# Kernel optimization log

Hardware: AMD Instinct MI355X
Metric: run time of the kernel (lower is better)

Reference implementation:

```python
import jax, jax.numpy as jnp
import numpy as np

B, S, D = 2, 1024, 2048
H, DN, DR, DV, R = 16, 128, 64, 128, 512
E, K, FI, SI = 12, 4, 1408, 2816
THETA = 10000.0
EPS = 1e-6


def rmsnorm(x, w):
    return x * jax.lax.rsqrt(jnp.mean(x * x, -1, keepdims=True) + EPS) * w


def rope(x, cos, sin):
    # interleaved-pair rotation (torch view_as_complex convention)
    x1, x2 = x[..., 0::2], x[..., 1::2]
    return jnp.stack([x1 * cos - x2 * sin, x1 * sin + x2 * cos], axis=-1).reshape(x.shape)


def setup_inputs() -> dict:
    key = jax.random.key(0)
    ks = jax.random.split(key, 16)
    w = lambda k, sh: jax.random.normal(k, sh, jnp.float32) * 0.02
    inp = {
        'x': jax.random.normal(ks[0], (B, S, D), jnp.float32),
        'wq': w(ks[1], (D, H * (DN + DR))),
        'wkv_a': w(ks[2], (D, R + DR)),
        'kv_norm_w': jnp.ones((R,), jnp.float32),
        'wkv_b': w(ks[3], (R, H * (DN + DV))),
        'wo': w(ks[4], (H * DV, D)),
        'norm_w': jnp.ones((D,), jnp.float32),
        'gate_w': w(ks[5], (D, E)),
        'gate_b': jnp.zeros((E,), jnp.float32),
        'w1': w(ks[6], (E, D, FI)),
        'w2': w(ks[7], (E, FI, D)),
        'w3': w(ks[8], (E, D, FI)),
        'ws1': w(ks[9], (D, SI)),
        'ws2': w(ks[10], (SI, D)),
        'ws3': w(ks[11], (D, SI)),
        'mask': jnp.triu(jnp.full((S, S), -1e9, jnp.float32), 1),  # causal
        'start_pos': 0,
    }
    return inp


def reference(x, wq, wkv_a, kv_norm_w, wkv_b, wo, norm_w, gate_w, gate_b,
              w1, w2, w3, ws1, ws2, ws3, mask, start_pos):
    def mla(h):
        q = (h @ wq).reshape(B, S, H, DN + DR)
        q_nope, q_pe = q[..., :DN], q[..., DN:]
        kv = h @ wkv_a                              # [B,S,R+DR]
        kv_lat = rmsnorm(kv[..., :R], kv_norm_w)    # latent KV (kv_lora_rank)
        k_pe = kv[..., R:]                          # [B,S,DR] shared across heads
        kvb = (kv_lat @ wkv_b).reshape(B, S, H, DN + DV)
        k_nope, v = kvb[..., :DN], kvb[..., DN:]
        pos = start_pos + jnp.arange(S)
        inv = 1.0 / (THETA ** (jnp.arange(0, DR, 2, dtype=jnp.float32) / DR))
        ang = pos[:, None].astype(jnp.float32) * inv[None, :]
        cos, sin = jnp.cos(ang), jnp.sin(ang)       # [S, DR//2]
        q_pe = rope(q_pe, cos[None, :, None, :], sin[None, :, None, :])
        k_pe = rope(k_pe, cos[None, :, :], sin[None, :, :])
        scale = (DN + DR) ** -0.5
        scores = (jnp.einsum('bshd,bthd->bhst', q_nope, k_nope)
                  + jnp.einsum('bshd,btd->bhst', q_pe, k_pe)) * scale
        scores = scores + mask[None, None, :, :]
        p = jax.nn.softmax(scores, axis=-1)
        o = jnp.einsum('bhst,bthd->bshd', p, v).reshape(B, S, H * DV)
        return o @ wo

    def moe(h):
        t = h.reshape(-1, D)                        # [T, D]
        T = t.shape[0]
        s = jax.nn.sigmoid(t @ gate_w)              # routing scores [T, E]
        _, topi = jax.lax.top_k(s + gate_b[None, :], K)   # adaptive bias only for selection
        wgt = jnp.take_along_axis(s, topi, axis=1)
        wgt = wgt / jnp.sum(wgt, -1, keepdims=True)
        route = jnp.zeros((T, E), t.dtype).at[jnp.arange(T)[:, None], topi].set(wgt)
        hh = jnp.einsum('td,edi->eti', t, w1)
        gg = jax.nn.silu(hh) * jnp.einsum('td,edi->eti', t, w3)
        eo = jnp.einsum('eti,eid->etd', gg, w2)
        out = jnp.einsum('te,etd->td', route, eo)
        shared = (jax.nn.silu(t @ ws1) * (t @ ws3)) @ ws2
        return (out + shared).reshape(B, S, D)

    first = mla(rmsnorm(x, norm_w)) + x
    return moe(rmsnorm(first, norm_w)) + first
```

## Files before the change

### kernel.cpp

```cpp
#include <hip/hip_runtime.h>
#include <math.h>

typedef unsigned short u16;
typedef __attribute__((ext_vector_type(8))) short short8;
typedef __attribute__((ext_vector_type(8))) _Float16 half8;
typedef __attribute__((ext_vector_type(4))) float f32x4;

__device__ inline u16 f32_to_bf16_rne(float f){
    unsigned int u = __float_as_uint(f);
    unsigned int r = (u + 0x7FFFu + ((u >> 16) & 1u)) >> 16;
    return (u16)r;
}
__device__ inline float bf16_to_f32(u16 h){ return __uint_as_float(((unsigned int)h) << 16); }
__device__ inline u16 h2b(_Float16 h){ union { _Float16 f; u16 u; } x; x.f = h; return x.u; }

__device__ __forceinline__ void glds16(const void* g, void* l){
    __builtin_amdgcn_global_load_lds((const __attribute__((address_space(1))) void*)g,
                                     (__attribute__((address_space(3))) void*)l, 16, 0, 0);
}
#define WAIT_VM0()  { asm volatile("s_waitcnt vmcnt(0)" ::: "memory"); __builtin_amdgcn_sched_barrier(0); }
#define WAIT_LGKM0() { asm volatile("s_waitcnt lgkmcnt(0)" ::: "memory"); __builtin_amdgcn_sched_barrier(0); }
#define RAW_BAR()   { __builtin_amdgcn_s_barrier(); __builtin_amdgcn_sched_barrier(0); }

#define TT 2048
#define DD 2048
#define SS 1024
#define NH 16

#define EPI_F32     0
#define EPI_BF16    1
#define EPI_RES     2
#define EPI_SILUMUL 3
#define EPI_F16PAIR 4
#define EPI_QROPE   5

template<int PAIR>
__global__ __launch_bounds__(256) void cvtT_k(const float* __restrict__ W, long long wstr,
        u16* __restrict__ WTh, u16* __restrict__ WTl, long long tstr, int K, int Nsrc){
    __shared__ float L[64][65];
    int e = blockIdx.z;
    const float* Wp = W + (long long)e * wstr;
    int k0 = blockIdx.y * 64, n0 = blockIdx.x * 64;
    int tid = threadIdx.x;
#pragma unroll
    for (int it = 0; it < 4; ++it) {
        int r = (tid >> 4) + it * 16, cc = (tid & 15) * 4;
        int col = n0 + cc;
        float4 v = {0.f, 0.f, 0.f, 0.f};
        if (col + 3 < Nsrc) v = *(const float4*)(Wp + (long long)(k0 + r) * Nsrc + col);
        else {
            const float* p = Wp + (long long)(k0 + r) * Nsrc;
            float tmp[4] = {0.f, 0.f, 0.f, 0.f};
#pragma unroll
            for (int q2 = 0; q2 < 4; q2++) if (col + q2 < Nsrc) tmp[q2] = p[col + q2];
            v.x = tmp[0]; v.y = tmp[1]; v.z = tmp[2]; v.w = tmp[3];
        }
        L[r][cc] = v.x; L[r][cc+1] = v.y; L[r][cc+2] = v.z; L[r][cc+3] = v.w;
    }
    __syncthreads();
#pragma unroll
    for (int it = 0; it < 2; ++it) {
        int idx = it * 256 + tid; int n = idx >> 3, kc = (idx & 7) * 8;
        u16 hi[8], lo[8];
#pragma unroll
        for (int u = 0; u < 8; ++u) {
            float v = L[kc + u][n];
            if (PAIR) { _Float16 h = (_Float16)v; hi[u] = h2b(h); lo[u] = h2b((_Float16)(v - (float)h)); }
            else hi[u] = f32_to_bf16_rne(v);
        }
        long long o = (long long)e * tstr + (long long)(n0 + n) * K + k0 + kc;
        *(short8*)(WTh + o) = *(short8*)hi;
        if (PAIR) *(short8*)(WTl + o) = *(short8*)lo;
    }
}

template<int EPI, bool PREC, bool AGLDS>
__global__ __launch_bounds__(256) void gemm_k(
    const u16* __restrict__ A0, const u16* __restrict__ A1, int lda,
    const u16* __restrict__ BTh, const u16* __restrict__ BTl, long long btstr,
    int M, int N, int K,
    const int* offs, const int* cnt, const int* gather, int ebase,
    void* C0, void* C1, int ldc,
    const void* aux, const float* __restrict__ cosT, const float* __restrict__ sinT)
{
    __shared__ u16 AsH[2][4096];
    __shared__ u16 AsL[PREC ? 2 : 1][PREC ? 4096 : 8];
    __shared__ u16 BsH[2][4096];
    __shared__ u16 BsL[PREC ? 2 : 1][PREC ? 4096 : 8];

    int tid  = threadIdx.x;
    int lane = tid & 63;
    int wv   = tid >> 6;
    int wm = (wv >> 1) * 64, wn = (wv & 1) * 64;

    int Lid = blockIdx.y * gridDim.x + blockIdx.x;
    int jj  = Lid >> 3;
    int yb  = jj % gridDim.y;
    int nb  = (Lid & 7) + ((jj / gridDim.y) << 3);
    int n0 = nb * 128;
    if (n0 >= N) return;

    int e    = ebase + blockIdx.z;
    int base = offs ? offs[e] : 0;
    int mc   = cnt ? cnt[e] : M;
    int m0   = yb * 128;
    if (m0 >= mc) return;
    const u16* Bh = BTh + (long long)blockIdx.z * btstr;
    const u16* Bl = PREC ? (BTl + (long long)blockIdx.z * btstr) : (const u16*)nullptr;

    int rr_ = tid >> 2, s4 = tid & 3;
    long long arow0 = -1, arow1 = -1;
    if (!AGLDS) {
        if (m0 + rr_ < mc)      arow0 = gather ? (long long)gather[base + m0 + rr_]      : (long long)(base + m0 + rr_);
        if (m0 + rr_ + 64 < mc) arow1 = gather ? (long long)gather[base + m0 + rr_ + 64] : (long long)(base + m0 + rr_ + 64);
    }

    f32x4 acc[4][4];
#pragma unroll
    for (int i = 0; i < 4; i++)
#pragma unroll
        for (int j = 0; j < 4; j++) { f32x4 z = {0.f,0.f,0.f,0.f}; acc[i][j] = z; }

    short8 zer = {0,0,0,0,0,0,0,0};
    short8 a0h = zer, a1h = zer, a0l = zer, a1l = zer;

    int gr0 = wv * 16 + (lane >> 2);
    int gsl = lane & 3;

#define STAGE_GL(PB, KT)                                                         \
    {                                                                            \
        _Pragma("unroll")                                                        \
        for (int it = 0; it < 2; ++it) {                                         \
            int r = it * 64 + gr0;                                               \
            int s = gsl ^ ((r >> 1) & 3);                                        \
            glds16(Bh + (long long)(n0 + r) * K + (KT) + s * 8,                  \
                   (char*)&BsH[PB][0] + it * 4096 + wv * 1024);                  \
            if (PREC)                                                            \
                glds16(Bl + (long long)(n0 + r) * K + (KT) + s * 8,              \
                       (char*)&BsL[PB][0] + it * 4096 + wv * 1024);              \
            if (AGLDS) {                                                         \
                glds16(A0 + (long long)(base + m0 + r) * lda + (KT) + s * 8,     \
                       (char*)&AsH[PB][0] + it * 4096 + wv * 1024);              \
                if (PREC)                                                        \
                    glds16(A1 + (long long)(base + m0 + r) * lda + (KT) + s * 8, \
                           (char*)&AsL[PB][0] + it * 4096 + wv * 1024);          \
            }                                                                    \
        }                                                                        \
        if (!AGLDS) {                                                            \
            a0h = (arow0 >= 0) ? *(const short8*)(A0 + arow0 * lda + (KT) + s4 * 8) : zer; \
            a1h = (arow1 >= 0) ? *(const short8*)(A0 + arow1 * lda + (KT) + s4 * 8) : zer; \
            if (PREC) {                                                          \
                a0l = (arow0 >= 0) ? *(const short8*)(A1 + arow0 * lda + (KT) + s4 * 8) : zer; \
                a1l = (arow1 >= 0) ? *(const short8*)(A1 + arow1 * lda + (KT) + s4 * 8) : zer; \
            }                                                                    \
        }                                                                        \
    }

    int pb = 0;
    STAGE_GL(0, 0);
    for (int kt = 0; kt < K; kt += 32) {
        WAIT_VM0();
        if (!AGLDS) {
            int d0 = rr_ * 64 + 16 * (s4 ^ ((rr_ >> 1) & 3));
            int r1w = rr_ + 64;
            int d1 = r1w * 64 + 16 * (s4 ^ ((r1w >> 1) & 3));
            *(short8*)((char*)&AsH[pb][0] + d0) = a0h;
            *(short8*)((char*)&AsH[pb][0] + d1) = a1h;
            if (PREC) {
                *(short8*)((char*)&AsL[pb][0] + d0) = a0l;
                *(short8*)((char*)&AsL[pb][0] + d1) = a1l;
            }
            WAIT_LGKM0();
        }
        RAW_BAR();
        if (kt + 32 < K) { STAGE_GL(pb ^ 1, kt + 32); }
        if (PREC) {
            half8 ah[4], al[4];
#pragma unroll
            for (int i = 0; i < 4; i++) {
                int ra = wm + i * 16 + (lane & 15);
                int off = ra * 64 + 16 * ((lane >> 4) ^ ((ra >> 1) & 3));
                ah[i] = *(const half8*)((const char*)&AsH[pb][0] + off);
                al[i] = *(const half8*)((const char*)&AsL[pb][0] + off);
            }
#pragma unroll
            for (int j = 0; j < 4; j++) {
                int rb = wn + j * 16 + (lane & 15);
                int off = rb * 64 + 16 * ((lane >> 4) ^ ((rb >> 1) & 3));
                half8 bh = *(const half8*)((const char*)&BsH[pb][0] + off);
                half8 bl = *(const half8*)((const char*)&BsL[pb][0] + off);
#pragma unroll
                for (int i = 0; i < 4; i++) {
                    acc[i][j] = __builtin_amdgcn_mfma_f32_16x16x32_f16(ah[i], bh, acc[i][j], 0, 0, 0);
                    acc[i][j] = __builtin_amdgcn_mfma_f32_16x16x32_f16(ah[i], bl, acc[i][j], 0, 0, 0);
                    acc[i][j] = __builtin_amdgcn_mfma_f32_16x16x32_f16(al[i], bh, acc[i][j], 0, 0, 0);
                }
            }
        } else {
            short8 af[4];
#pragma unroll
            for (int i = 0; i < 4; i++) {
                int ra = wm + i * 16 + (lane & 15);
                af[i] = *(const short8*)((const char*)&AsH[pb][0] + ra * 64 + 16 * ((lane >> 4) ^ ((ra >> 1) & 3)));
            }
#pragma unroll
            for (int j = 0; j < 4; j++) {
                int rb = wn + j * 16 + (lane & 15);
                short8 bfr = *(const short8*)((const char*)&BsH[pb][0] + rb * 64 + 16 * ((lane >> 4) ^ ((rb >> 1) & 3)));
#pragma unroll
                for (int i = 0; i < 4; i++)
                    acc[i][j] = __builtin_amdgcn_mfma_f32_16x16x32_bf16(af[i], bfr, acc[i][j], 0, 0, 0);
            }
        }
        pb ^= 1;
    }
#undef STAGE_GL

    if (EPI == EPI_QROPE) {
#pragma unroll
        for (int i = 0; i < 4; i++) {
            int rr0 = m0 + wm + i * 16 + ((lane >> 4) << 2);
#pragma unroll
            for (int j = 0; j < 4; j++) {
                int col = n0 + wn + j * 16 + (lane & 15);
                int hd = col % 192;
#pragma unroll
                for (int r = 0; r < 4; r++) {
                    int rr = rr0 + r;
                    float v = acc[i][j][r];
                    float pv = __shfl_xor(v, 1);
                    float outv = v;
                    if (hd >= 128) {
                        int s = rr & (SS - 1);
                        int pi2 = (hd - 128) >> 1;
                        float cc_ = cosT[s * 32 + pi2], sn_ = sinT[s * 32 + pi2];
                        bool odd = col & 1;
                        float a0 = odd ? pv : v, a1 = odd ? v : pv;
                        outv = odd ? (a0 * sn_ + a1 * cc_) : (a0 * cc_ - a1 * sn_);
                    }
                    long long cidx = (long long)rr * ldc + col;
                    _Float16 hh = (_Float16)outv;
                    ((u16*)C0)[cidx] = h2b(hh);
                    ((u16*)C1)[cidx] = h2b((_Float16)(outv - (float)hh));
                }
            }
        }
    } else {
#pragma unroll
        for (int i = 0; i < 4; i++) {
            int rbase = m0 + wm + i * 16 + ((lane >> 4) << 2);
#pragma unroll
            for (int j = 0; j < 4; j++) {
                int col = n0 + wn + j * 16 + (lane & 15);
                if (col >= N) continue;
#pragma unroll
                for (int r = 0; r < 4; r++) {
                    int rr = rbase + r;
                    if (rr >= mc) continue;
                    long long cidx = (long long)(base + rr) * ldc + col;
                    float v = acc[i][j][r];
                    if (EPI == EPI_F32)      ((float*)C0)[cidx] = v;
                    else if (EPI == EPI_BF16) ((u16*)C0)[cidx] = f32_to_bf16_rne(v);
                    else if (EPI == EPI_RES)  ((float*)C0)[cidx] = v + ((const float*)aux)[cidx];
                    else if (EPI == EPI_SILUMUL) {
                        float h1v = bf16_to_f32(((const u16*)aux)[cidx]);
                        float g = h1v / (1.f + __expf(-h1v)) * v;
                        ((u16*)C0)[cidx] = f32_to_bf16_rne(g);
                    } else {
                        _Float16 hh = (_Float16)v;
                        ((u16*)C0)[cidx] = h2b(hh);
                        ((u16*)C1)[cidx] = h2b((_Float16)(v - (float)hh));
                    }
                }
            }
        }
    }
}

__global__ void costab_k(const int* sp, float* ct, float* st){
    int idx = blockIdx.x * 256 + threadIdx.x;
    if (idx >= SS * 32) return;
    int i = idx & 31, s = idx >> 5;
    float inv = powf(10000.0f, -(float)i / 32.0f);
    float a = (float)(sp[0] + s) * inv;
    ct[idx] = cosf(a);
    st[idx] = sinf(a);
}

template<int MODE>
__global__ __launch_bounds__(256) void rms_k(const float* __restrict__ x, const float* __restrict__ w,
                                             u16* o0, u16* o1){
    int t = blockIdx.x, tid = threadIdx.x;
    const float* row = x + (long long)t * DD;
    float4 v0 = *(const float4*)(row + tid * 4);
    float4 v1 = *(const float4*)(row + 1024 + tid * 4);
    float ss = v0.x*v0.x + v0.y*v0.y + v0.z*v0.z + v0.w*v0.w
             + v1.x*v1.x + v1.y*v1.y + v1.z*v1.z + v1.w*v1.w;
#pragma unroll
    for (int d = 1; d < 64; d <<= 1) ss += __shfl_xor(ss, d, 64);
    __shared__ float red[4];
    if ((tid & 63) == 0) red[tid >> 6] = ss;
    __syncthreads();
    float sc = rsqrtf((red[0] + red[1] + red[2] + red[3]) / (float)DD + 1e-6f);
    float a[8];
    a[0]=v0.x; a[1]=v0.y; a[2]=v0.z; a[3]=v0.w; a[4]=v1.x; a[5]=v1.y; a[6]=v1.z; a[7]=v1.w;
#pragma unroll
    for (int q2 = 0; q2 < 8; q2++) {
        int d = (q2 < 4) ? (tid * 4 + q2) : (1024 + tid * 4 + (q2 - 4));
        float y = a[q2] * sc * w[d];
        if (MODE == 0) {
            _Float16 hh = (_Float16)y;
            o0[(long long)t * DD + d] = h2b(hh);
            o1[(long long)t * DD + d] = h2b((_Float16)(y - (float)hh));
        } else {
            o0[(long long)t * DD + d] = f32_to_bf16_rne(y);
        }
    }
}

__global__ __launch_bounds__(256) void kvprep_k(const float* __restrict__ kv, const float* __restrict__ kw,
    const float* __restrict__ ct, const float* __restrict__ st,
    u16* lath, u16* latl, u16* kpeh, u16* kpel){
    int t = blockIdx.x, tid = threadIdx.x;
    const float* row = kv + (long long)t * 576;
    float x0 = row[tid], x1 = row[256 + tid];
    float ss = x0 * x0 + x1 * x1;
#pragma unroll
    for (int d = 1; d < 64; d <<= 1) ss += __shfl_xor(ss, d, 64);
    __shared__ float red[4];
    if ((tid & 63) == 0) red[tid >> 6] = ss;
    __syncthreads();
    float sc = rsqrtf((red[0] + red[1] + red[2] + red[3]) / 512.f + 1e-6f);
    float y0 = x0 * sc * kw[tid], y1 = x1 * sc * kw[256 + tid];
    _Float16 h0 = (_Float16)y0, h1 = (_Float16)y1;
    lath[(long long)t * 512 + tid] = h2b(h0);
    latl[(long long)t * 512 + tid] = h2b((_Float16)(y0 - (float)h0));
    lath[(long long)t * 512 + 256 + tid] = h2b(h1);
    latl[(long long)t * 512 + 256 + tid] = h2b((_Float16)(y1 - (float)h1));
    if (tid < 32) {
        int s = t & (SS - 1);
        float a0 = row[512 + 2 * tid], a1 = row[513 + 2 * tid];
        float c = ct[s * 32 + tid], sn = st[s * 32 + tid];
        float r0 = a0 * c - a1 * sn, r1 = a0 * sn + a1 * c;
        _Float16 p0 = (_Float16)r0, p1 = (_Float16)r1;
        kpeh[(long long)t * 64 + 2 * tid]     = h2b(p0);
        kpel[(long long)t * 64 + 2 * tid]     = h2b((_Float16)(r0 - (float)p0));
        kpeh[(long long)t * 64 + 2 * tid + 1] = h2b(p1);
        kpel[(long long)t * 64 + 2 * tid + 1] = h2b((_Float16)(r1 - (float)p1));
    }
}

__global__ __launch_bounds__(256) void vtprep_k(const u16* __restrict__ kvbh, const u16* __restrict__ kvbl,
                                                u16* vth, u16* vtl){
    __shared__ u16 L[64][136];
    int bh = blockIdx.x, st = blockIdx.y, pl = blockIdx.z;
    const u16* src = pl ? kvbl : kvbh;
    u16* dst = pl ? vtl : vth;
    int b = bh >> 4, hh = bh & 15;
    int tid = threadIdx.x;
#pragma unroll
    for (int it = 0; it < 4; ++it) {
        int idx = it * 256 + tid; int sl = idx >> 4, dc = idx & 15;
        long long t = (long long)b * SS + st * 64 + sl;
        *(short8*)&L[sl][dc * 8] = *(const short8*)(src + t * 4096 + hh * 256 + 128 + dc * 8);
    }
    __syncthreads();
#pragma unroll
    for (int it = 0; it < 4; ++it) {
        int idx = it * 256 + tid; int d = idx >> 3, sc = idx & 7;
        short8 v;
#pragma unroll
        for (int u = 0; u < 8; u++) v[u] = (short)L[sc * 8 + u][d];
        *(short8*)(dst + ((long long)bh * 128 + d) * SS + st * 64 + sc * 8) = v;
    }
}

__global__ __launch_bounds__(256) void attn_k(
    const u16* __restrict__ qh_, const u16* __restrict__ ql_,
    const u16* __restrict__ kvbh, const u16* __restrict__ kvbl,
    const u16* __restrict__ kpeh, const u16* __restrict__ kpel,
    const u16* __restrict__ vth, const u16* __restrict__ vtl,
    u16* ohi, u16* olo)
{
    __shared__ u16 KsH[32][200], KsL[32][200];
    __shared__ u16 VsH[128][40], VsL[128][40];
    __shared__ u16 PlH[4][16][40], PlL[4][16][40];
    int bx = blockIdx.x, bh = blockIdx.y;
    int qi = (bh & 16) ? bx : (15 - bx);
    int b = bh >> 4, h = bh & 15;
    int tid = threadIdx.x, lane = tid & 63, wv = tid >> 6;
    int q0 = qi * 64;
    const u16* vbh = vth + (long long)bh * 128 * SS;
    const u16* vbl = vtl + (long long)bh * 128 * SS;

    half8 qh[6], ql[6];
    {
        int row = q0 + wv * 16 + (lane & 15);
        const u16* ph = qh_ + (long long)(b * SS + row) * 3072 + h * 192 + (lane >> 4) * 8;
        const u16* pl = ql_ + (long long)(b * SS + row) * 3072 + h * 192 + (lane >> 4) * 8;
#pragma unroll
        for (int ks = 0; ks < 6; ks++) {
            qh[ks] = *(const half8*)(ph + ks * 32);
            ql[ks] = *(const half8*)(pl + ks * 32);
        }
    }
    float mrun[4], lrun[4];
    f32x4 oacc[8];
#pragma unroll
    for (int r = 0; r < 4; r++) { mrun[r] = -1e30f; lrun[r] = 0.f; }
#pragma unroll
    for (int f = 0; f < 8; f++) { f32x4 z = {0.f,0.f,0.f,0.f}; oacc[f] = z; }
    const float scale = 0.07216878364870322f;

    short8 kh0, kh1, kh2, kl0, kl1, kl2, vh0, vh1, vl0, vl1;
    int kr0 = tid / 24 + 0,  kc0 = tid % 24;
    int kr1 = (256 + tid) / 24, kc1 = (256 + tid) % 24;
    int kr2 = (512 + tid) / 24, kc2 = (512 + tid) % 24;
    int vr0 = tid >> 2, vc0 = tid & 3;
    int vr1 = (256 + tid) >> 2, vc1 = vc0;

#define ALOAD(T0)                                                                   \
    {                                                                               \
        long long tg0 = (long long)b * SS + (T0);                                   \
        if (kc0 < 16) { kh0 = *(const short8*)(kvbh + (tg0 + kr0) * 4096 + h * 256 + kc0 * 8); \
                        kl0 = *(const short8*)(kvbl + (tg0 + kr0) * 4096 + h * 256 + kc0 * 8); } \
        else          { kh0 = *(const short8*)(kpeh + (tg0 + kr0) * 64 + (kc0 - 16) * 8);      \
                        kl0 = *(const short8*)(kpel + (tg0 + kr0) * 64 + (kc0 - 16) * 8); }    \
        if (kc1 < 16) { kh1 = *(const short8*)(kvbh + (tg0 + kr1) * 4096 + h * 256 + kc1 * 8); \
                        kl1 = *(const short8*)(kvbl + (tg0 + kr1) * 4096 + h * 256 + kc1 * 8); } \
        else          { kh1 = *(const short8*)(kpeh + (tg0 + kr1) * 64 + (kc1 - 16) * 8);      \
                        kl1 = *(const short8*)(kpel + (tg0 + kr1) * 64 + (kc1 - 16) * 8); }    \
        if (kc2 < 16) { kh2 = *(const short8*)(kvbh + (tg0 + kr2) * 4096 + h * 256 + kc2 * 8); \
                        kl2 = *(const short8*)(kvbl + (tg0 + kr2) * 4096 + h * 256 + kc2 * 8); } \
        else          { kh2 = *(const short8*)(kpeh + (tg0 + kr2) * 64 + (kc2 - 16) * 8);      \
                        kl2 = *(const short8*)(kpel + (tg0 + kr2) * 64 + (kc2 - 16) * 8); }    \
        vh0 = *(const short8*)(vbh + (long long)vr0 * SS + (T0) + vc0 * 8);         \
        vl0 = *(const short8*)(vbl + (long long)vr0 * SS + (T0) + vc0 * 8);         \
        vh1 = *(const short8*)(vbh + (long long)vr1 * SS + (T0) + vc1 * 8);         \
        vl1 = *(const short8*)(vbl + (long long)vr1 * SS + (T0) + vc1 * 8);         \
    }

    int ntile = 2 * qi + 2;
    ALOAD(0);
    for (int ti = 0; ti < ntile; ++ti) {
        int t0 = ti * 32;
        WAIT_VM0();
        RAW_BAR();
        *(short8*)&KsH[kr0][kc0 * 8] = kh0; *(short8*)&KsL[kr0][kc0 * 8] = kl0;
        *(short8*)&KsH[kr1][kc1 * 8] = kh1; *(short8*)&KsL[kr1][kc1 * 8] = kl1;
        *(short8*)&KsH[kr2][kc2 * 8] = kh2; *(short8*)&KsL[kr2][kc2 * 8] = kl2;
        *(short8*)&VsH[vr0][vc0 * 8] = vh0; *(short8*)&VsL[vr0][vc0 * 8] = vl0;
        *(short8*)&VsH[vr1][vc1 * 8] = vh1; *(short8*)&VsL[vr1][vc1 * 8] = vl1;
        WAIT_LGKM0();
        RAW_BAR();
        if (ti + 1 < ntile) ALOAD(t0 + 32);
        f32x4 s[2];
#pragma unroll
        for (int nt = 0; nt < 2; ++nt) {
            f32x4 a = {0.f,0.f,0.f,0.f};
#pragma unroll
            for (int ks = 0; ks < 6; ++ks) {
                half8 kh = *(const half8*)&KsH[nt * 16 + (lane & 15)][ks * 32 + (lane >> 4) * 8];
                half8 kl = *(const half8*)&KsL[nt * 16 + (lane & 15)][ks * 32 + (lane >> 4) * 8];
                a = __builtin_amdgcn_mfma_f32_16x16x32_f16(qh[ks], kh, a, 0, 0, 0);
                a = __builtin_amdgcn_mfma_f32_16x16x32_f16(qh[ks], kl, a, 0, 0, 0);
                a = __builtin_amdgcn_mfma_f32_16x16x32_f16(ql[ks], kh, a, 0, 0, 0);
            }
            s[nt] = a;
        }
#pragma unroll
        for (int nt = 0; nt < 2; ++nt)
#pragma unroll
            for (int r = 0; r < 4; ++r) {
                float v = s[nt][r] * scale;
                if (ti >= 2 * qi) {
                    int t = t0 + nt * 16 + (lane & 15);
                    int sq = q0 + wv * 16 + (lane >> 4) * 4 + r;
                    if (t > sq) v = -1e30f;
                }
                s[nt][r] = v;
            }
        float corr[4];
#pragma unroll
        for (int r = 0; r < 4; ++r) {
            float m = fmaxf(s[0][r], s[1][r]);
#pragma unroll
            for (int d = 1; d < 16; d <<= 1) m = fmaxf(m, __shfl_xor(m, d, 64));
            float mn = fmaxf(mrun[r], m);
            corr[r] = __expf(mrun[r] - mn);
            mrun[r] = mn;
        }
        float rs[4] = {0.f, 0.f, 0.f, 0.f};
#pragma unroll
        for (int nt = 0; nt < 2; ++nt)
#pragma unroll
            for (int r = 0; r < 4; ++r) {
                float p = __expf(s[nt][r] - mrun[r]);
                s[nt][r] = p;
                rs[r] += p;
            }
#pragma unroll
        for (int r = 0; r < 4; ++r) {
            float tsum = rs[r];
#pragma unroll
            for (int d = 1; d < 16; d <<= 1) tsum += __shfl_xor(tsum, d, 64);
            lrun[r] = lrun[r] * corr[r] + tsum;
        }
#pragma unroll
        for (int f = 0; f < 8; f++)
#pragma unroll
            for (int r = 0; r < 4; r++) oacc[f][r] *= corr[r];
#pragma unroll
        for (int nt = 0; nt < 2; ++nt)
#pragma unroll
            for (int r = 0; r < 4; ++r) {
                float p = s[nt][r];
                _Float16 ph = (_Float16)p;
                PlH[wv][(lane >> 4) * 4 + r][nt * 16 + (lane & 15)] = h2b(ph);
                PlL[wv][(lane >> 4) * 4 + r][nt * 16 + (lane & 15)] = h2b((_Float16)(p - (float)ph));
            }
        half8 pfh = *(const half8*)&PlH[wv][lane & 15][(lane >> 4) * 8];
        half8 pfl = *(const half8*)&PlL[wv][lane & 15][(lane >> 4) * 8];
#pragma unroll
        for (int f = 0; f < 8; ++f) {
            half8 vh = *(const half8*)&VsH[f * 16 + (lane & 15)][(lane >> 4) * 8];
            half8 vl = *(const half8*)&VsL[f * 16 + (lane & 15)][(lane >> 4) * 8];
            oacc[f] = __builtin_amdgcn_mfma_f32_16x16x32_f16(pfh, vh, oacc[f], 0, 0, 0);
            oacc[f] = __builtin_amdgcn_mfma_f32_16x16x32_f16(pfh, vl, oacc[f], 0, 0, 0);
            oacc[f] = __builtin_amdgcn_mfma_f32_16x16x32_f16(pfl, vh, oacc[f], 0, 0, 0);
        }
    }
#undef ALOAD
#pragma unroll
    for (int f = 0; f < 8; ++f)
#pragma unroll
        for (int r = 0; r < 4; ++r) {
            int sq = q0 + wv * 16 + (lane >> 4) * 4 + r;
            float v = oacc[f][r] / lrun[r];
            _Float16 hh = (_Float16)v;
            long long o = ((long long)(b * SS + sq)) * 2048 + h * 128 + f * 16 + (lane & 15);
            ohi[o] = h2b(hh);
            olo[o] = h2b((_Float16)(v - (float)hh));
        }
}

__global__ __launch_bounds__(256) void gate_k(const float* __restrict__ first,
    const float* __restrict__ nw, const float* __restrict__ gw, const float* __restrict__ gb,
    int* topi, float* wgt){
    int wv = threadIdx.x >> 6, lane = threadIdx.x & 63;
    int t = blockIdx.x * 4 + wv;
    const float* row = first + (long long)t * DD;
    float rv[32];
    float ss = 0.f;
#pragma unroll
    for (int it = 0; it < 32; ++it) {
        float v = row[it * 64 + lane];
        rv[it] = v;
        ss += v * v;
    }
#pragma unroll
    for (int d = 1; d < 64; d <<= 1) ss += __shfl_xor(ss, d, 64);
    float sc = rsqrtf(ss / (float)DD + 1e-6f);
    float acc[12];
#pragma unroll
    for (int e = 0; e < 12; e++) acc[e] = 0.f;
#pragma unroll
    for (int it = 0; it < 32; ++it) {
        int i = it * 64 + lane;
        float v = rv[it] * sc * nw[i];
        const float* g = gw + (long long)i * 12;
        float4 g0 = *(const float4*)g;
        float4 g1 = *(const float4*)(g + 4);
        float4 g2 = *(const float4*)(g + 8);
        acc[0] += v * g0.x; acc[1] += v * g0.y; acc[2]  += v * g0.z; acc[3]  += v * g0.w;
        acc[4] += v * g1.x; acc[5] += v * g1.y; acc[6]  += v * g1.z; acc[7]  += v * g1.w;
        acc[8] += v * g2.x; acc[9] += v * g2.y; acc[10] += v * g2.z; acc[11] += v * g2.w;
    }
#pragma unroll
    for (int e = 0; e < 12; e++)
#pragma unroll
        for (int d = 1; d < 64; d <<= 1) acc[e] += __shfl_xor(acc[e], d, 64);
    if (lane == 0) {
        float s[12], rank[12];
#pragma unroll
        for (int e = 0; e < 12; e++) { s[e] = 1.f / (1.f + expf(-acc[e])); rank[e] = s[e] + gb[e]; }
        int sel[4]; float wv4[4]; float wsum = 0.f;
#pragma unroll
        for (int k = 0; k < 4; k++) {
            int bi = 0; float bv = -1e30f;
#pragma unroll
            for (int e = 0; e < 12; e++) if (rank[e] > bv) { bv = rank[e]; bi = e; }
            sel[k] = bi; rank[bi] = -1e31f;
            wv4[k] = s[bi]; wsum += s[bi];
        }
#pragma unroll
        for (int k = 0; k < 4; k++) {
            topi[t * 4 + k] = sel[k];
            wgt[t * 4 + k] = wv4[k] / wsum;
        }
    }
}

__global__ __launch_bounds__(256) void offs_k(const int* __restrict__ topi,
                                              int* cnt, int* offs, int* cur){
    __shared__ int lh[4][12];
    int tid = threadIdx.x, wv = tid >> 6, lane = tid & 63;
    int c[12];
#pragma unroll
    for (int e = 0; e < 12; e++) c[e] = 0;
    for (int i = tid; i < TT * 4; i += 256) {
        int e = topi[i];
#pragma unroll
        for (int q = 0; q < 12; q++) c[q] += (e == q) ? 1 : 0;
    }
#pragma unroll
    for (int e = 0; e < 12; e++) {
        int v = c[e];
#pragma unroll
        for (int d = 1; d < 64; d <<= 1) v += __shfl_xor(v, d, 64);
        if (lane == 0) lh[wv][e] = v;
    }
    __syncthreads();
    if (tid == 0) {
        int a = 0;
        for (int e = 0; e < 12; e++) {
            int tot = lh[0][e] + lh[1][e] + lh[2][e] + lh[3][e];
            cnt[e] = tot; offs[e] = a; a += tot; cur[e] = 0;
        }
        offs[12] = a;
    }
}

__global__ __launch_bounds__(256) void scatter_k(const int* __restrict__ topi,
    const float* __restrict__ wgt, const int* __restrict__ offs,
    int* cur, int* tok, float* wgl, int* posm){
    __shared__ int lh[12];
    __shared__ int gb[12];
    int tid = threadIdx.x;
    if (tid < 12) lh[tid] = 0;
    __syncthreads();
    int t = blockIdx.x * 256 + tid;
    int e4[4], lr[4];
#pragma unroll
    for (int k = 0; k < 4; k++) {
        e4[k] = topi[t * 4 + k];
        lr[k] = atomicAdd(&lh[e4[k]], 1);
    }
    __syncthreads();
    if (tid < 12) gb[tid] = atomicAdd(&cur[tid], lh[tid]);
    __syncthreads();
#pragma unroll
    for (int k = 0; k < 4; k++) {
        int pos = offs[e4[k]] + gb[e4[k]] + lr[k];
        tok[pos] = t;
        wgl[pos] = wgt[t * 4 + k];
        posm[t * 4 + k] = pos;
    }
}

__global__ void final_k(const float* __restrict__ first, const u16* __restrict__ so,
    const u16* __restrict__ eo, const int* __restrict__ posm, const float* __restrict__ wgl,
    float* out){
    int idx = blockIdx.x * 256 + threadIdx.x;
    int d4 = idx & 511, t = idx >> 9;
    int d = d4 * 4;
    const float* fp = first + (long long)t * DD + d;
    const u16* sp = so + (long long)t * DD + d;
    float r0 = fp[0] + bf16_to_f32(sp[0]);
    float r1 = fp[1] + bf16_to_f32(sp[1]);
    float r2 = fp[2] + bf16_to_f32(sp[2]);
    float r3 = fp[3] + bf16_to_f32(sp[3]);
#pragma unroll
    for (int k = 0; k < 4; k++) {
        int pos = posm[t * 4 + k];
        float wv = wgl[pos];
        const u16* ep = eo + (long long)pos * DD + d;
        r0 += wv * bf16_to_f32(ep[0]);
        r1 += wv * bf16_to_f32(ep[1]);
        r2 += wv * bf16_to_f32(ep[2]);
        r3 += wv * bf16_to_f32(ep[3]);
    }
    float4 res = {r0, r1, r2, r3};
    *(float4*)(out + (long long)t * DD + d) = res;
}

extern "C" void kernel_launch(void* const* d_in, const int* in_sizes, int n_in,
                              void* d_out, int out_size, void* d_ws, size_t ws_size,
                              hipStream_t stream)
{
    const float* x       = (const float*)d_in[0];
    const float* wq      = (const float*)d_in[1];
    const float* wkv_a   = (const float*)d_in[2];
    const float* kvnw    = (const float*)d_in[3];
    const float* wkv_b   = (const float*)d_in[4];
    const float* wo      = (const float*)d_in[5];
    const float* norm_w  = (const float*)d_in[6];
    const float* gate_w  = (const float*)d_in[7];
    const float* gate_b  = (const float*)d_in[8];
    const float* w1      = (const float*)d_in[9];
    const float* w2      = (const float*)d_in[10];
    const float* w3      = (const float*)d_in[11];
    const float* ws1     = (const float*)d_in[12];
    const float* ws2     = (const float*)d_in[13];
    const float* ws3     = (const float*)d_in[14];
    const int*   startp  = (const int*)d_in[16];
    char* ws = (char*)d_ws;

    const size_t O_COS = 0, O_SIN = 131072, O_KPEH = 262144, O_KPEL = 524288;
    const size_t O_TOPI = 786432, O_WGT = 819200, O_TOK = 851968, O_WGL = 884736, O_POSM = 917504;
    const size_t O_CNT = 950272, O_OFFS = 950336, O_CUR = 950400;
    const size_t O_WB = 1048576;
    const size_t B2 = 26214400;
    const size_t O_H    = B2,             O_HLO  = B2 + 8388608;
    const size_t O_Q    = B2 + 16777216,  O_QLO  = B2 + 29360128;
    const size_t O_KVF  = B2 + 41943040;
    const size_t O_LATH = B2 + 46661632,  O_LATL = B2 + 48758784;
    const size_t O_KVBH = B2 + 50855936,  O_KVBL = B2 + 67633152;
    const size_t O_VTH  = B2,             O_VTL  = B2 + 8388608;
    const size_t O_OH   = B2 + 84410368,  O_OL   = B2 + 92798976;
    const size_t O_FIRST= B2 + 16777216;
    const size_t O_TBF  = B2;
    const size_t O_H1   = B2 + 33554432;
    const size_t O_EO   = B2 + 56623104;
    const size_t O_SH1  = B2 + 90177536;
    const size_t O_SO   = B2 + 101711872;

    float* cosT = (float*)(ws + O_COS);  float* sinT = (float*)(ws + O_SIN);
    u16* kpeh = (u16*)(ws + O_KPEH);     u16* kpel = (u16*)(ws + O_KPEL);
    int* topi = (int*)(ws + O_TOPI);     float* wgt = (float*)(ws + O_WGT);
    int* tok = (int*)(ws + O_TOK);       float* wgl = (float*)(ws + O_WGL);
    int* posm = (int*)(ws + O_POSM);
    int* cntp = (int*)(ws + O_CNT); int* offsp = (int*)(ws + O_OFFS); int* curp = (int*)(ws + O_CUR);
    u16* WB   = (u16*)(ws + O_WB);
    u16* hhi = (u16*)(ws + O_H);    u16* hlo = (u16*)(ws + O_HLO);
    u16* qhp = (u16*)(ws + O_Q);    u16* qlp = (u16*)(ws + O_QLO);
    float* kvf = (float*)(ws + O_KVF);
    u16* lath = (u16*)(ws + O_LATH); u16* latl = (u16*)(ws + O_LATL);
    u16* kvbh = (u16*)(ws + O_KVBH); u16* kvbl = (u16*)(ws + O_KVBL);
    u16* vth = (u16*)(ws + O_VTH);  u16* vtl = (u16*)(ws + O_VTL);
    u16* oh  = (u16*)(ws + O_OH);   u16* ol  = (u16*)(ws + O_OL);
    float* first = (float*)(ws + O_FIRST);
    u16* tbf = (u16*)(ws + O_TBF);
    u16* h1buf = (u16*)(ws + O_H1); u16* eo = (u16*)(ws + O_EO);
    u16* sh1 = (u16*)(ws + O_SH1);  u16* sobuf = (u16*)(ws + O_SO);

    costab_k<<<128, 256, 0, stream>>>(startp, cosT, sinT);
    rms_k<0><<<TT, 256, 0, stream>>>(x, norm_w, hhi, hlo);

    cvtT_k<1><<<dim3(48, 32, 1), 256, 0, stream>>>(wq, 0, WB, WB + 6291456, 0, 2048, 3072);
    gemm_k<EPI_QROPE, true, true><<<dim3(24, 16, 1), 256, 0, stream>>>(
        hhi, hlo, 2048, WB, WB + 6291456, 0, 2048, 3072, 2048,
        nullptr, nullptr, nullptr, 0, qhp, qlp, 3072, nullptr, cosT, sinT);

    cvtT_k<1><<<dim3(10, 32, 1), 256, 0, stream>>>(wkv_a, 0, WB, WB + 1310720, 0, 2048, 576);
    gemm_k<EPI_F32, true, true><<<dim3(8, 16, 1), 256, 0, stream>>>(
        hhi, hlo, 2048, WB, WB + 1310720, 0, 2048, 576, 2048,
        nullptr, nullptr, nullptr, 0, kvf, nullptr, 576, nullptr, nullptr, nullptr);
    kvprep_k<<<TT, 256, 0, stream>>>(kvf, kvnw, cosT, sinT, lath, latl, kpeh, kpel);

    cvtT_k<1><<<dim3(64, 8, 1), 256, 0, stream>>>(wkv_b, 0, WB, WB + 2097152, 0, 512, 4096);
    gemm_k<EPI_F16PAIR, true, true><<<dim3(32, 16, 1), 256, 0, stream>>>(
        lath, latl, 512, WB, WB + 2097152, 0, 2048, 4096, 512,
        nullptr, nullptr, nullptr, 0, kvbh, kvbl, 4096, nullptr, nullptr, nullptr);

    vtprep_k<<<dim3(32, 16, 2), 256, 0, stream>>>(kvbh, kvbl, vth, vtl);
    attn_k<<<dim3(16, 32, 1), 256, 0, stream>>>(qhp, qlp, kvbh, kvbl, kpeh, kpel, vth, vtl, oh, ol);

    cvtT_k<1><<<dim3(32, 32, 1), 256, 0, stream>>>(wo, 0, WB, WB + 4194304, 0, 2048, 2048);
    gemm_k<EPI_RES, true, true><<<dim3(16, 16, 1), 256, 0, stream>>>(
        oh, ol, 2048, WB, WB + 4194304, 0, 2048, 2048, 2048,
        nullptr, nullptr, nullptr, 0, first, nullptr, 2048, x, nullptr, nullptr);

    rms_k<1><<<TT, 256, 0, stream>>>(first, norm_w, tbf, nullptr);
    gate_k<<<512, 256, 0, stream>>>(first, norm_w, gate_w, gate_b, topi, wgt);
    offs_k<<<1, 256, 0, stream>>>(topi, cntp, offsp, curp);
    scatter_k<<<8, 256, 0, stream>>>(topi, wgt, offsp, curp, tok, wgl, posm);

    const long long EW = (long long)2048 * 1408;
    for (int g = 0; g < 3; ++g) {
        cvtT_k<0><<<dim3(22, 32, 4), 256, 0, stream>>>(w1 + (long long)g * 4 * EW, EW, WB, nullptr, EW, 2048, 1408);
        gemm_k<EPI_BF16, false, false><<<dim3(16, 16, 4), 256, 0, stream>>>(
            tbf, nullptr, 2048, WB, nullptr, EW, 2048, 1408, 2048,
            offsp, cntp, tok, 4 * g, h1buf, nullptr, 1408, nullptr, nullptr, nullptr);
        cvtT_k<0><<<dim3(22, 32, 4), 256, 0, stream>>>(w3 + (long long)g * 4 * EW, EW, WB, nullptr, EW, 2048, 1408);
        gemm_k<EPI_SILUMUL, false, false><<<dim3(16, 16, 4), 256, 0, stream>>>(
            tbf, nullptr, 2048, WB, nullptr, EW, 2048, 1408, 2048,
            offsp, cntp, tok, 4 * g, h1buf, nullptr, 1408, h1buf, nullptr, nullptr);
        cvtT_k<0><<<dim3(32, 22, 4), 256, 0, stream>>>(w2 + (long long)g * 4 * EW, EW, WB, nullptr, EW, 1408, 2048);
        gemm_k<EPI_BF16, false, true><<<dim3(16, 16, 4), 256, 0, stream>>>(
            h1buf, nullptr, 1408, WB, nullptr, EW, 2048, 2048, 1408,
            offsp, cntp, nullptr, 4 * g, eo, nullptr, 2048, nullptr, nullptr, nullptr);
    }

    cvtT_k<0><<<dim3(44, 32, 1), 256, 0, stream>>>(ws1, 0, WB, nullptr, 0, 2048, 2816);
    gemm_k<EPI_BF16, false, true><<<dim3(24, 16, 1), 256, 0, stream>>>(
        tbf, nullptr, 2048, WB, nullptr, 0, 2048, 2816, 2048,
        nullptr, nullptr, nullptr, 0, sh1, nullptr, 2816, nullptr, nullptr, nullptr);
    cvtT_k<0><<<dim3(44, 32, 1), 256, 0, stream>>>(ws3, 0, WB, nullptr, 0, 2048, 2816);
    gemm_k<EPI_SILUMUL, false, true><<<dim3(24, 16, 1), 256, 0, stream>>>(
        tbf, nullptr, 2048, WB, nullptr, 0, 2048, 2816, 2048,
        nullptr, nullptr, nullptr, 0, sh1, nullptr, 2816, sh1, nullptr, nullptr);
    cvtT_k<0><<<dim3(32, 44, 1), 256, 0, stream>>>(ws2, 0, WB, nullptr, 0, 2816, 2048);
    gemm_k<EPI_BF16, false, true><<<dim3(16, 16, 1), 256, 0, stream>>>(
        sh1, nullptr, 2816, WB, nullptr, 0, 2048, 2048, 2816,
        nullptr, nullptr, nullptr, 0, sobuf, nullptr, 2048, nullptr, nullptr, nullptr);

    final_k<<<4096, 256, 0, stream>>>(first, sobuf, eo, posm, wgl, (float*)d_out);
}
```

Measured before the change: 1.373 ms.

## Load GEMM A fragments directly from global into registers, dropping A LDS staging

The GEMM kernel no longer stages the A tile in shared memory. Each lane now loads its MFMA A fragments (rows wm+i*16+lane&15, 8-element k chunk) straight from global memory every k-step, with gather and row-bound masking folded into precomputed offsets. Only B stays double-buffered via global_load_lds. This removes the A LDS writes and reads and shrinks shared memory, which could raise occupancy. In exchange, the A loads are no longer prefetched a stage ahead, are issued right after the barrier, and are redundant across the two waves that share the same rows, so global/L2 traffic rises and load latency may be exposed.

```diff
diff --git a/kernel.cpp b/kernel.cpp
--- a/kernel.cpp
+++ b/kernel.cpp
@@ -74,7 +74,7 @@
     }
 }
 
-template<int EPI, bool PREC, bool AGLDS>
+template<int EPI, bool PREC, bool GATHER>
 __global__ __launch_bounds__(256) void gemm_k(
     const u16* __restrict__ A0, const u16* __restrict__ A1, int lda,
     const u16* __restrict__ BTh, const u16* __restrict__ BTl, long long btstr,
@@ -83,8 +83,6 @@
     void* C0, void* C1, int ldc,
     const void* aux, const float* __restrict__ cosT, const float* __restrict__ sinT)
 {
-    __shared__ u16 AsH[2][4096];
-    __shared__ u16 AsL[PREC ? 2 : 1][PREC ? 4096 : 8];
     __shared__ u16 BsH[2][4096];
     __shared__ u16 BsL[PREC ? 2 : 1][PREC ? 4096 : 8];
 
@@ -108,11 +106,17 @@
     const u16* Bh = BTh + (long long)blockIdx.z * btstr;
     const u16* Bl = PREC ? (BTl + (long long)blockIdx.z * btstr) : (const u16*)nullptr;
 
-    int rr_ = tid >> 2, s4 = tid & 3;
-    long long arow0 = -1, arow1 = -1;
-    if (!AGLDS) {
-        if (m0 + rr_ < mc)      arow0 = gather ? (long long)gather[base + m0 + rr_]      : (long long)(base + m0 + rr_);
-        if (m0 + rr_ + 64 < mc) arow1 = gather ? (long long)gather[base + m0 + rr_ + 64] : (long long)(base + m0 + rr_ + 64);
+    long long aoff[4];
+    bool aok[4];
+#pragma unroll
+    for (int i = 0; i < 4; i++) {
+        int row = m0 + wm + i * 16 + (lane & 15);
+        bool ok = row < mc;
+        long long rowg;
+        if (GATHER) { int gi = ok ? (base + row) : 0; rowg = (long long)gather[gi]; }
+        else        { rowg = ok ? (long long)(base + row) : 0; }
+        aoff[i] = rowg * (long long)lda + ((lane >> 4) * 8);
+        aok[i] = ok;
     }
 
     f32x4 acc[4][4];
@@ -120,14 +124,11 @@
     for (int i = 0; i < 4; i++)
 #pragma unroll
         for (int j = 0; j < 4; j++) { f32x4 z = {0.f,0.f,0.f,0.f}; acc[i][j] = z; }
-
-    short8 zer = {0,0,0,0,0,0,0,0};
-    short8 a0h = zer, a1h = zer, a0l = zer, a1l = zer;
 
     int gr0 = wv * 16 + (lane >> 2);
     int gsl = lane & 3;
 
-#define STAGE_GL(PB, KT)                                                         \
+#define STAGE_B(PB, KT)                                                          \
     {                                                                            \
         _Pragma("unroll")                                                        \
         for (int it = 0; it < 2; ++it) {                                         \
@@ -138,51 +139,37 @@
             if (PREC)                                                            \
                 glds16(Bl + (long long)(n0 + r) * K + (KT) + s * 8,              \
                        (char*)&BsL[PB][0] + it * 4096 + wv * 1024);              \
-            if (AGLDS) {                                                         \
-                glds16(A0 + (long long)(base + m0 + r) * lda + (KT) + s * 8,     \
-                       (char*)&AsH[PB][0] + it * 4096 + wv * 1024);              \
-                if (PREC)                                                        \
-                    glds16(A1 + (long long)(base + m0 + r) * lda + (KT) + s * 8, \
-                           (char*)&AsL[PB][0] + it * 4096 + wv * 1024);          \
-            }                                                                    \
         }                                                                        \
-        if (!AGLDS) {                                                            \
-            a0h = (arow0 >= 0) ? *(const short8*)(A0 + arow0 * lda + (KT) + s4 * 8) : zer; \
-            a1h = (arow1 >= 0) ? *(const short8*)(A0 + arow1 * lda + (KT) + s4 * 8) : zer; \
-            if (PREC) {                                                          \
-                a0l = (arow0 >= 0) ? *(const short8*)(A1 + arow0 * lda + (KT) + s4 * 8) : zer; \
-                a1l = (arow1 >= 0) ? *(const short8*)(A1 + arow1 * lda + (KT) + s4 * 8) : zer; \
-            }                                                                    \
-        }                                                                        \
     }
 
     int pb = 0;
-    STAGE_GL(0, 0);
+    STAGE_B(0, 0);
     for (int kt = 0; kt < K; kt += 32) {
         WAIT_VM0();
-        if (!AGLDS) {
-            int d0 = rr_ * 64 + 16 * (s4 ^ ((rr_ >> 1) & 3));
-            int r1w = rr_ + 64;
-            int d1 = r1w * 64 + 16 * (s4 ^ ((r1w >> 1) & 3));
-            *(short8*)((char*)&AsH[pb][0] + d0) = a0h;
-            *(short8*)((char*)&AsH[pb][0] + d1) = a1h;
-            if (PREC) {
-                *(short8*)((char*)&AsL[pb][0] + d0) = a0l;
-                *(short8*)((char*)&AsL[pb][0] + d1) = a1l;
-            }
-            WAIT_LGKM0();
-        }
         RAW_BAR();
-        if (kt + 32 < K) { STAGE_GL(pb ^ 1, kt + 32); }
+        half8 ah[4], al[4];
+        short8 af[4];
         if (PREC) {
-            half8 ah[4], al[4];
+            half8 hz = {(_Float16)0,(_Float16)0,(_Float16)0,(_Float16)0,
+                        (_Float16)0,(_Float16)0,(_Float16)0,(_Float16)0};
 #pragma unroll
             for (int i = 0; i < 4; i++) {
-                int ra = wm + i * 16 + (lane & 15);
-                int off = ra * 64 + 16 * ((lane >> 4) ^ ((ra >> 1) & 3));
-                ah[i] = *(const half8*)((const char*)&AsH[pb][0] + off);
-                al[i] = *(const half8*)((const char*)&AsL[pb][0] + off);
-            }
+                half8 v = *(const half8*)(A0 + aoff[i] + kt);
+                half8 w = *(const half8*)(A1 + aoff[i] + kt);
+                ah[i] = aok[i] ? v : hz;
+                al[i] = aok[i] ? w : hz;
+            }
+        } else {
+            short8 zer = {0,0,0,0,0,0,0,0};
+#pragma unroll
+            for (int i = 0; i < 4; i++) {
+                short8 v = *(const short8*)(A0 + aoff[i] + kt);
+                af[i] = aok[i] ? v : zer;
+            }
+        }
+        __builtin_amdgcn_sched_barrier(0);
+        if (kt + 32 < K) { STAGE_B(pb ^ 1, kt + 32); }
+        if (PREC) {
 #pragma unroll
             for (int j = 0; j < 4; j++) {
                 int rb = wn + j * 16 + (lane & 15);
@@ -197,12 +184,6 @@
                 }
             }
         } else {
-            short8 af[4];
-#pragma unroll
-            for (int i = 0; i < 4; i++) {
-                int ra = wm + i * 16 + (lane & 15);
-                af[i] = *(const short8*)((const char*)&AsH[pb][0] + ra * 64 + 16 * ((lane >> 4) ^ ((ra >> 1) & 3)));
-            }
 #pragma unroll
             for (int j = 0; j < 4; j++) {
                 int rb = wn + j * 16 + (lane & 15);
@@ -214,7 +195,7 @@
         }
         pb ^= 1;
     }
-#undef STAGE_GL
+#undef STAGE_B
 
     if (EPI == EPI_QROPE) {
 #pragma unroll
@@ -748,18 +729,18 @@
     rms_k<0><<<TT, 256, 0, stream>>>(x, norm_w, hhi, hlo);
 
     cvtT_k<1><<<dim3(48, 32, 1), 256, 0, stream>>>(wq, 0, WB, WB + 6291456, 0, 2048, 3072);
-    gemm_k<EPI_QROPE, true, true><<<dim3(24, 16, 1), 256, 0, stream>>>(
+    gemm_k<EPI_QROPE, true, false><<<dim3(24, 16, 1), 256, 0, stream>>>(
         hhi, hlo, 2048, WB, WB + 6291456, 0, 2048, 3072, 2048,
         nullptr, nullptr, nullptr, 0, qhp, qlp, 3072, nullptr, cosT, sinT);
 
     cvtT_k<1><<<dim3(10, 32, 1), 256, 0, stream>>>(wkv_a, 0, WB, WB + 1310720, 0, 2048, 576);
-    gemm_k<EPI_F32, true, true><<<dim3(8, 16, 1), 256, 0, stream>>>(
+    gemm_k<EPI_F32, true, false><<<dim3(8, 16, 1), 256, 0, stream>>>(
         hhi, hlo, 2048, WB, WB + 1310720, 0, 2048, 576, 2048,
         nullptr, nullptr, nullptr, 0, kvf, nullptr, 576, nullptr, nullptr, nullptr);
     kvprep_k<<<TT, 256, 0, stream>>>(kvf, kvnw, cosT, sinT, lath, latl, kpeh, kpel);
 
     cvtT_k<1><<<dim3(64, 8, 1), 256, 0, stream>>>(wkv_b, 0, WB, WB + 2097152, 0, 512, 4096);
-    gemm_k<EPI_F16PAIR, true, true><<<dim3(32, 16, 1), 256, 0, stream>>>(
+    gemm_k<EPI_F16PAIR, true, false><<<dim3(32, 16, 1), 256, 0, stream>>>(
         lath, latl, 512, WB, WB + 2097152, 0, 2048, 4096, 512,
         nullptr, nullptr, nullptr, 0, kvbh, kvbl, 4096, nullptr, nullptr, nullptr);
 
@@ -767,7 +748,7 @@
     attn_k<<<dim3(16, 32, 1), 256, 0, stream>>>(qhp, qlp, kvbh, kvbl, kpeh, kpel, vth, vtl, oh, ol);
 
     cvtT_k<1><<<dim3(32, 32, 1), 256, 0, stream>>>(wo, 0, WB, WB + 4194304, 0, 2048, 2048);
-    gemm_k<EPI_RES, true, true><<<dim3(16, 16, 1), 256, 0, stream>>>(
+    gemm_k<EPI_RES, true, false><<<dim3(16, 16, 1), 256, 0, stream>>>(
         oh, ol, 2048, WB, WB + 4194304, 0, 2048, 2048, 2048,
         nullptr, nullptr, nullptr, 0, first, nullptr, 2048, x, nullptr, nullptr);
 
@@ -779,29 +760,29 @@
     const long long EW = (long long)2048 * 1408;
     for (int g = 0; g < 3; ++g) {
         cvtT_k<0><<<dim3(22, 32, 4), 256, 0, stream>>>(w1 + (long long)g * 4 * EW, EW, WB, nullptr, EW, 2048, 1408);
-        gemm_k<EPI_BF16, false, false><<<dim3(16, 16, 4), 256, 0, stream>>>(
+        gemm_k<EPI_BF16, false, true><<<dim3(16, 16, 4), 256, 0, stream>>>(
             tbf, nullptr, 2048, WB, nullptr, EW, 2048, 1408, 2048,
             offsp, cntp, tok, 4 * g, h1buf, nullptr, 1408, nullptr, nullptr, nullptr);
         cvtT_k<0><<<dim3(22, 32, 4), 256, 0, stream>>>(w3 + (long long)g * 4 * EW, EW, WB, nullptr, EW, 2048, 1408);
-        gemm_k<EPI_SILUMUL, false, false><<<dim3(16, 16, 4), 256, 0, stream>>>(
+        gemm_k<EPI_SILUMUL, false, true><<<dim3(16, 16, 4), 256, 0, stream>>>(
             tbf, nullptr, 2048, WB, nullptr, EW, 2048, 1408, 2048,
             offsp, cntp, tok, 4 * g, h1buf, nullptr, 1408, h1buf, nullptr, nullptr);
         cvtT_k<0><<<dim3(32, 22, 4), 256, 0, stream>>>(w2 + (long long)g * 4 * EW, EW, WB, nullptr, EW, 1408, 2048);
-        gemm_k<EPI_BF16, false, true><<<dim3(16, 16, 4), 256, 0, stream>>>(
+        gemm_k<EPI_BF16, false, false><<<dim3(16, 16, 4), 256, 0, stream>>>(
             h1buf, nullptr, 1408, WB, nullptr, EW, 2048, 2048, 1408,
             offsp, cntp, nullptr, 4 * g, eo, nullptr, 2048, nullptr, nullptr, nullptr);
     }
 
     cvtT_k<0><<<dim3(44, 32, 1), 256, 0, stream>>>(ws1, 0, WB, nullptr, 0, 2048, 2816);
-    gemm_k<EPI_BF16, false, true><<<dim3(24, 16, 1), 256, 0, stream>>>(
+    gemm_k<EPI_BF16, false, false><<<dim3(24, 16, 1), 256, 0, stream>>>(
         tbf, nullptr, 2048, WB, nullptr, 0, 2048, 2816, 2048,
         nullptr, nullptr, nullptr, 0, sh1, nullptr, 2816, nullptr, nullptr, nullptr);
     cvtT_k<0><<<dim3(44, 32, 1), 256, 0, stream>>>(ws3, 0, WB, nullptr, 0, 2048, 2816);
-    gemm_k<EPI_SILUMUL, false, true><<<dim3(24, 16, 1), 256, 0, stream>>>(
+    gemm_k<EPI_SILUMUL, false, false><<<dim3(24, 16, 1), 256, 0, stream>>>(
         tbf, nullptr, 2048, WB, nullptr, 0, 2048, 2816, 2048,
         nullptr, nullptr, nullptr, 0, sh1, nullptr, 2816, sh1, nullptr, nullptr);
     cvtT_k<0><<<dim3(32, 44, 1), 256, 0, stream>>>(ws2, 0, WB, nullptr, 0, 2816, 2048);
-    gemm_k<EPI_BF16, false, true><<<dim3(16, 16, 1), 256, 0, stream>>>(
+    gemm_k<EPI_BF16, false, false><<<dim3(16, 16, 1), 256, 0, stream>>>(
         sh1, nullptr, 2816, WB, nullptr, 0, 2048, 2048, 2816,
         nullptr, nullptr, nullptr, 0, sobuf, nullptr, 2048, nullptr, nullptr, nullptr);
 
```

Measured after the change: 2.071 ms. 50.9% more time.
